# Kernel tuning notes

Hardware: AMD Instinct MI355X
Metric: run time of the kernel (lower is better)

The kernel has to match this reference:

```python
import jax, jax.numpy as jnp
import numpy as np

SEQ, D_IN, D_OUT = 4096, 1024, 1024


def setup_inputs() -> dict:
    key = jax.random.key(0)
    kx, kq, kk, kv = jax.random.split(key, 4)
    x = jax.random.normal(kx, (SEQ, D_IN), dtype=jnp.float32)
    # original uses torch.rand (uniform [0,1)) for parameter init
    W_query = jax.random.uniform(kq, (D_IN, D_OUT), dtype=jnp.float32)
    W_key = jax.random.uniform(kk, (D_IN, D_OUT), dtype=jnp.float32)
    W_value = jax.random.uniform(kv, (D_IN, D_OUT), dtype=jnp.float32)
    return {"x": x, "W_query": W_query, "W_key": W_key, "W_value": W_value}


def reference(x, W_query, W_key, W_value):
    queries = x @ W_query          # [S, d_out]
    keys = x @ W_key               # [S, d_out]
    values = x @ W_value           # [S, d_out]
    scale = keys.shape[-1] ** 0.5
    attn_scores = queries @ keys.T # [S, S]
    attn_weights = jax.nn.softmax(attn_scores / scale, axis=-1)
    context_vec = attn_weights @ values  # [S, d_out]
    return context_vec
```

## Files before the change

kernel.cpp:

```cpp
#include <hip/hip_runtime.h>
#include <stdint.h>

#define SEQ 4096
#define DM 1024

typedef __attribute__((ext_vector_type(8))) short short8;
typedef __attribute__((ext_vector_type(4))) float f32x4;
typedef unsigned short ushort_t;

__device__ inline ushort_t f2bf(float f) {
  union { float f; uint32_t u; } v; v.f = f;
  return (ushort_t)((v.u + 0x7FFFu + ((v.u >> 16) & 1u)) >> 16);
}
__device__ inline float bf2f(ushort_t h) {
  union { uint32_t u; float f; } v; v.u = ((uint32_t)h) << 16;
  return v.f;
}

__device__ inline void async_copy16(const void* g, void* lds) {
  __builtin_amdgcn_global_load_lds(
      (const __attribute__((address_space(1))) uint32_t*)g,
      (__attribute__((address_space(3))) uint32_t*)lds, 16, 0, 0);
}


__global__ __launch_bounds__(256, 3)
void gemm_qkv(const ushort_t* __restrict__ A, const ushort_t* __restrict__ Bt,
              ushort_t* __restrict__ Qb, ushort_t* __restrict__ Kb,
              ushort_t* __restrict__ Vb) {
  __shared__ ushort_t As[2][128 * 32];
  __shared__ ushort_t Bs[2][128 * 32];
  const int t = threadIdx.x;
  const int wave = t >> 6, lane = t & 63;
  const int quad = lane >> 4, l16 = lane & 15;
  const int m0 = blockIdx.y * 128, n0 = blockIdx.x * 128;
  const bool is_v = (n0 >= 2048);
  const int wm = (wave & 1) * 64, wn = (wave >> 1) * 64;
  const int srow = lane >> 2;
  const int sf = (srow >> 1) & 3;
  const int gcol = (((lane & 3) - sf) & 3) * 8;
  const int rf = (l16 >> 1) & 3;
  const int aslot = ((quad + rf) & 3) * 8;

  f32x4 acc[4][4] = {};

  for (int k0 = 0; k0 < 1024; k0 += 32) {
#pragma unroll
    for (int i = 0; i < 2; ++i) {
      int c = wave * 2 + i;
      const ushort_t* ga = A + (size_t)(m0 + c * 16 + srow) * 2048 + k0 + gcol;
      const ushort_t* gb = Bt + (size_t)(n0 + c * 16 + srow) * 2048 + k0 + gcol;
      async_copy16(ga, As[0] + c * 512);
      async_copy16(gb, Bs[0] + c * 512);
      if (!is_v) {
        async_copy16(ga + 1024, As[1] + c * 512);
        async_copy16(gb + 1024, Bs[1] + c * 512);
      }
    }
    __syncthreads();
    short8 a[4], b[4], x[4];
#pragma unroll
    for (int i = 0; i < 4; ++i) {
      a[i] = *(const short8*)(As[0] + (wm + i * 16 + l16) * 32 + aslot);
      b[i] = *(const short8*)(Bs[0] + (wn + i * 16 + l16) * 32 + aslot);
    }
#pragma unroll
    for (int i = 0; i < 4; ++i)
#pragma unroll
      for (int j = 0; j < 4; ++j)
        acc[i][j] = __builtin_amdgcn_mfma_f32_16x16x32_bf16(a[i], b[j], acc[i][j], 0, 0, 0);
    if (!is_v) {
#pragma unroll
      for (int j = 0; j < 4; ++j)
        x[j] = *(const short8*)(Bs[1] + (wn + j * 16 + l16) * 32 + aslot);
#pragma unroll
      for (int i = 0; i < 4; ++i)
#pragma unroll
        for (int j = 0; j < 4; ++j)
          acc[i][j] = __builtin_amdgcn_mfma_f32_16x16x32_bf16(a[i], x[j], acc[i][j], 0, 0, 0);
#pragma unroll
      for (int i = 0; i < 4; ++i)
        x[i] = *(const short8*)(As[1] + (wm + i * 16 + l16) * 32 + aslot);
#pragma unroll
      for (int i = 0; i < 4; ++i)
#pragma unroll
        for (int j = 0; j < 4; ++j)
          acc[i][j] = __builtin_amdgcn_mfma_f32_16x16x32_bf16(x[i], b[j], acc[i][j], 0, 0, 0);
    }
    __syncthreads();
  }

  if (is_v) {
    const int cb = n0 - 2048;
#pragma unroll
    for (int i = 0; i < 4; ++i)
#pragma unroll
      for (int j = 0; j < 4; ++j)
#pragma unroll
        for (int r = 0; r < 4; ++r) {
          int row = m0 + wm + i * 16 + quad * 4 + r;
          int col = cb + wn + j * 16 + l16;
          Vb[(size_t)row * 1024 + col] = f2bf(acc[i][j][r]);
        }
  } else {
    ushort_t* Cm = (n0 < 1024) ? Qb : Kb;
    const int cb = n0 & 1023;
#pragma unroll
    for (int i = 0; i < 4; ++i)
#pragma unroll
      for (int j = 0; j < 4; ++j)
#pragma unroll
        for (int r = 0; r < 4; ++r) {
          int row = m0 + wm + i * 16 + quad * 4 + r;
          int col = cb + wn + j * 16 + l16;
          float v = acc[i][j][r];
          ushort_t h = f2bf(v);
          size_t base = (size_t)row * 2048 + col;
          Cm[base] = h;
          Cm[base + 1024] = f2bf(v - bf2f(h));
        }
  }
}

__global__ __launch_bounds__(256, 3)
void gemm_sc(const ushort_t* __restrict__ A, const ushort_t* __restrict__ Bt,
             float* __restrict__ C, float scale) {
  const int id = blockIdx.x;
  const int rr = id & 7, w = (id >> 3) & 15, q = id >> 7;
  const int m0 = (q * 4 + (w >> 2)) * 128;
  const int n0 = (rr * 4 + (w & 3)) * 128;

  __shared__ ushort_t As[2][128 * 32];
  __shared__ ushort_t Bs[2][128 * 32];
  const int t = threadIdx.x;
  const int wave = t >> 6, lane = t & 63;
  const int quad = lane >> 4, l16 = lane & 15;
  const int wm = (wave & 1) * 64, wn = (wave >> 1) * 64;
  const int srow = lane >> 2;
  const int sf = (srow >> 1) & 3;
  const int gcol = (((lane & 3) - sf) & 3) * 8;
  const int rf = (l16 >> 1) & 3;
  const int aslot = ((quad + rf) & 3) * 8;

  f32x4 acc[4][4] = {};

  for (int k0 = 0; k0 < 1024; k0 += 32) {
#pragma unroll
    for (int i = 0; i < 2; ++i) {
      int c = wave * 2 + i;
      const ushort_t* ga = A + (size_t)(m0 + c * 16 + srow) * 2048 + k0 + gcol;
      const ushort_t* gb = Bt + (size_t)(n0 + c * 16 + srow) * 2048 + k0 + gcol;
      async_copy16(ga,        As[0] + c * 512);
      async_copy16(ga + 1024, As[1] + c * 512);
      async_copy16(gb,        Bs[0] + c * 512);
      async_copy16(gb + 1024, Bs[1] + c * 512);
    }
    __syncthreads();
    short8 a[4], b[4], x[4];
#pragma unroll
    for (int i = 0; i < 4; ++i) {
      a[i] = *(const short8*)(As[0] + (wm + i * 16 + l16) * 32 + aslot);
      b[i] = *(const short8*)(Bs[0] + (wn + i * 16 + l16) * 32 + aslot);
    }
#pragma unroll
    for (int i = 0; i < 4; ++i)
#pragma unroll
      for (int j = 0; j < 4; ++j)
        acc[i][j] = __builtin_amdgcn_mfma_f32_16x16x32_bf16(a[i], b[j], acc[i][j], 0, 0, 0);
#pragma unroll
    for (int j = 0; j < 4; ++j)
      x[j] = *(const short8*)(Bs[1] + (wn + j * 16 + l16) * 32 + aslot);
#pragma unroll
    for (int i = 0; i < 4; ++i)
#pragma unroll
      for (int j = 0; j < 4; ++j)
        acc[i][j] = __builtin_amdgcn_mfma_f32_16x16x32_bf16(a[i], x[j], acc[i][j], 0, 0, 0);
#pragma unroll
    for (int i = 0; i < 4; ++i)
      x[i] = *(const short8*)(As[1] + (wm + i * 16 + l16) * 32 + aslot);
#pragma unroll
    for (int i = 0; i < 4; ++i)
#pragma unroll
      for (int j = 0; j < 4; ++j)
        acc[i][j] = __builtin_amdgcn_mfma_f32_16x16x32_bf16(x[i], b[j], acc[i][j], 0, 0, 0);
    __syncthreads();
  }

#pragma unroll
  for (int i = 0; i < 4; ++i)
#pragma unroll
    for (int j = 0; j < 4; ++j)
#pragma unroll
      for (int r = 0; r < 4; ++r) {
        int row = m0 + wm + i * 16 + quad * 4 + r;
        int col = n0 + wn + j * 16 + l16;
        C[(size_t)row * SEQ + col] = acc[i][j][r] * scale;
      }
}

__global__ __launch_bounds__(256)
void gemm_pv(const ushort_t* __restrict__ P, const ushort_t* __restrict__ Vt,
             float* __restrict__ C) {
  const int id = blockIdx.x;
  const int g = ((id >> 6) << 3) | (id & 7);
  const int j = (id >> 3) & 7;
  const int z = g & 3, m = g >> 2;
  const int m0 = m * 128, n0 = j * 128, kbeg = z * 1024;

  __shared__ ushort_t As[128 * 32];
  __shared__ ushort_t Bs[128 * 32];
  const int t = threadIdx.x;
  const int wave = t >> 6, lane = t & 63;
  const int quad = lane >> 4, l16 = lane & 15;
  const int wm = (wave & 1) * 64, wn = (wave >> 1) * 64;
  const int srow = lane >> 2;
  const int sf = (srow >> 1) & 3;
  const int gcol = (((lane & 3) - sf) & 3) * 8;
  const int rf = (l16 >> 1) & 3;
  const int aslot = ((quad + rf) & 3) * 8;

  f32x4 acc[4][4] = {};
  for (int k0 = kbeg; k0 < kbeg + 1024; k0 += 32) {
#pragma unroll
    for (int i = 0; i < 2; ++i) {
      int c = wave * 2 + i;
      async_copy16(P + (size_t)(m0 + c * 16 + srow) * 4096 + k0 + gcol, As + c * 512);
      async_copy16(Vt + (size_t)(n0 + c * 16 + srow) * SEQ + k0 + gcol, Bs + c * 512);
    }
    __syncthreads();
    short8 a[4], b[4];
#pragma unroll
    for (int i = 0; i < 4; ++i) {
      a[i] = *(const short8*)(As + (wm + i * 16 + l16) * 32 + aslot);
      b[i] = *(const short8*)(Bs + (wn + i * 16 + l16) * 32 + aslot);
    }
#pragma unroll
    for (int i = 0; i < 4; ++i)
#pragma unroll
      for (int j2 = 0; j2 < 4; ++j2)
        acc[i][j2] = __builtin_amdgcn_mfma_f32_16x16x32_bf16(a[i], b[j2], acc[i][j2], 0, 0, 0);
    __syncthreads();
  }
#pragma unroll
  for (int i = 0; i < 4; ++i)
#pragma unroll
    for (int j2 = 0; j2 < 4; ++j2)
#pragma unroll
      for (int r = 0; r < 4; ++r) {
        int row = m0 + wm + i * 16 + quad * 4 + r;
        int col = n0 + wn + j2 * 16 + l16;
        atomicAdd(C + (size_t)row * DM + col, acc[i][j2][r]);
      }
}

__global__ __launch_bounds__(256)
void split_x(const float* __restrict__ x, ushort_t* __restrict__ Xp) {
  int idx = (blockIdx.x * 256 + threadIdx.x) * 4;
  int r = idx >> 10, c = idx & 1023;
  float4 v = *(const float4*)(x + idx);
  ushort4 hi, lo;
  hi.x = f2bf(v.x); lo.x = f2bf(v.x - bf2f(hi.x));
  hi.y = f2bf(v.y); lo.y = f2bf(v.y - bf2f(hi.y));
  hi.z = f2bf(v.z); lo.z = f2bf(v.z - bf2f(hi.z));
  hi.w = f2bf(v.w); lo.w = f2bf(v.w - bf2f(hi.w));
  *(ushort4*)(Xp + (size_t)r * 2048 + c) = hi;
  *(ushort4*)(Xp + (size_t)r * 2048 + 1024 + c) = lo;
}

__global__ __launch_bounds__(256)
void splitT_w(const float* __restrict__ W, ushort_t* __restrict__ Wp) {
  __shared__ float tile[64][65];
  const int bn = blockIdx.x * 64, bk = blockIdx.y * 64;
  const int tx = threadIdx.x & 63, ty = threadIdx.x >> 6;
#pragma unroll
  for (int i = ty; i < 64; i += 4)
    tile[i][tx] = W[(size_t)(bk + i) * DM + bn + tx];
  __syncthreads();
#pragma unroll
  for (int i = ty; i < 64; i += 4) {
    float v = tile[tx][i];
    ushort_t h = f2bf(v);
    Wp[(size_t)(bn + i) * 2048 + bk + tx] = h;
    Wp[(size_t)(bn + i) * 2048 + 1024 + bk + tx] = f2bf(v - bf2f(h));
  }
}

__global__ __launch_bounds__(256)
void transpose_bf16(const ushort_t* __restrict__ in, int istride,
                    ushort_t* __restrict__ out, int R) {
  __shared__ ushort_t tile[64][65];
  const int bc = blockIdx.x * 64, br = blockIdx.y * 64;
  const int tx = threadIdx.x & 63, ty = threadIdx.x >> 6;
#pragma unroll
  for (int i = ty; i < 64; i += 4)
    tile[i][tx] = in[(size_t)(br + i) * istride + bc + tx];
  __syncthreads();
#pragma unroll
  for (int i = ty; i < 64; i += 4)
    out[(size_t)(bc + i) * R + br + tx] = tile[tx][i];
}

__global__ __launch_bounds__(256)
void softmax_rows(const float* __restrict__ S, ushort_t* __restrict__ Pd) {
  const int row = blockIdx.x;
  const int t = threadIdx.x, lane = t & 63, wave = t >> 6;
  const float4* s4 = (const float4*)(S + (size_t)row * SEQ);
  float4 v[4];
  float m = -3.4e38f;
#pragma unroll
  for (int i = 0; i < 4; ++i) {
    v[i] = s4[i * 256 + t];
    m = fmaxf(m, fmaxf(fmaxf(v[i].x, v[i].y), fmaxf(v[i].z, v[i].w)));
  }
  __shared__ float redm[4], reds[4];
#pragma unroll
  for (int o = 32; o; o >>= 1) m = fmaxf(m, __shfl_xor(m, o));
  if (lane == 0) redm[wave] = m;
  __syncthreads();
  m = fmaxf(fmaxf(redm[0], redm[1]), fmaxf(redm[2], redm[3]));
  float sum = 0.f;
#pragma unroll
  for (int i = 0; i < 4; ++i) {
    v[i].x = __expf(v[i].x - m); v[i].y = __expf(v[i].y - m);
    v[i].z = __expf(v[i].z - m); v[i].w = __expf(v[i].w - m);
    sum += v[i].x + v[i].y + v[i].z + v[i].w;
  }
#pragma unroll
  for (int o = 32; o; o >>= 1) sum += __shfl_xor(sum, o);
  if (lane == 0) reds[wave] = sum;
  __syncthreads();
  const float inv = 1.f / (reds[0] + reds[1] + reds[2] + reds[3]);
  ushort4* p4 = (ushort4*)(Pd + (size_t)row * SEQ);
#pragma unroll
  for (int i = 0; i < 4; ++i) {
    ushort4 o;
    o.x = f2bf(v[i].x * inv); o.y = f2bf(v[i].y * inv);
    o.z = f2bf(v[i].z * inv); o.w = f2bf(v[i].w * inv);
    p4[i * 256 + t] = o;
  }
}

extern "C" void kernel_launch(void* const* d_in, const int* in_sizes, int n_in,
                              void* d_out, int out_size, void* d_ws, size_t ws_size,
                              hipStream_t stream) {
  const float* x  = (const float*)d_in[0];
  const float* Wq = (const float*)d_in[1];
  const float* Wk = (const float*)d_in[2];
  const float* Wv = (const float*)d_in[3];
  float* out = (float*)d_out;
  char* ws = (char*)d_ws;
  const size_t MB = (size_t)1 << 20;
  ushort_t* Xp   = (ushort_t*)(ws + 0 * MB);
  ushort_t* Wall = (ushort_t*)(ws + 16 * MB);
  ushort_t* Qb   = (ushort_t*)(ws + 28 * MB);
  ushort_t* Kb   = (ushort_t*)(ws + 44 * MB);
  ushort_t* Vb   = (ushort_t*)(ws + 60 * MB);
  ushort_t* VT   = (ushort_t*)(ws + 68 * MB);
  float*    S    = (float*)(ws + 76 * MB);
  ushort_t* Pd   = (ushort_t*)(ws + 0 * MB);

  hipMemsetAsync(d_out, 0, (size_t)SEQ * DM * sizeof(float), stream);

  split_x<<<SEQ * DM / 1024, 256, 0, stream>>>(x, Xp);
  splitT_w<<<dim3(16, 16), 256, 0, stream>>>(Wq, Wall + (size_t)0 * DM * 2048);
  splitT_w<<<dim3(16, 16), 256, 0, stream>>>(Wk, Wall + (size_t)1 * DM * 2048);
  splitT_w<<<dim3(16, 16), 256, 0, stream>>>(Wv, Wall + (size_t)2 * DM * 2048);

  gemm_qkv<<<dim3(3 * DM / 128, SEQ / 128), 256, 0, stream>>>(
      Xp, Wall, Qb, Kb, Vb);

  transpose_bf16<<<dim3(DM / 64, SEQ / 64), 256, 0, stream>>>(Vb, 1024, VT, SEQ);

  gemm_sc<<<1024, 256, 0, stream>>>(Qb, Kb, S, 0.03125f);

  softmax_rows<<<SEQ, 256, 0, stream>>>(S, Pd);

  gemm_pv<<<1024, 256, 0, stream>>>(Pd, VT, out);
}
```

Baseline: 364.3 us.

## Deepen PV k-tile to 64, merge weight split launches, simplify score-GEMM grid

The PV GEMM now stages 64-wide K tiles with an 8-slot XOR swizzle, so it does two MFMA sub-steps per barrier pair and needs half as many synchronizations. The three per-weight split/transpose launches are merged into a single launch using blockIdx.z. The score GEMM drops its swizzled block-to-tile mapping in favour of a plain 2D grid, which may lose L2 locality. The PV change doubles its LDS use per block, which could reduce occupancy.

```diff
diff --git a/kernel.cpp b/kernel.cpp
--- a/kernel.cpp
+++ b/kernel.cpp
@@ -125,10 +125,7 @@
 __global__ __launch_bounds__(256, 3)
 void gemm_sc(const ushort_t* __restrict__ A, const ushort_t* __restrict__ Bt,
              float* __restrict__ C, float scale) {
-  const int id = blockIdx.x;
-  const int rr = id & 7, w = (id >> 3) & 15, q = id >> 7;
-  const int m0 = (q * 4 + (w >> 2)) * 128;
-  const int n0 = (rr * 4 + (w & 3)) * 128;
+  const int m0 = blockIdx.y * 128, n0 = blockIdx.x * 128;
 
   __shared__ ushort_t As[2][128 * 32];
   __shared__ ushort_t Bs[2][128 * 32];
@@ -207,38 +204,42 @@
   const int z = g & 3, m = g >> 2;
   const int m0 = m * 128, n0 = j * 128, kbeg = z * 1024;
 
-  __shared__ ushort_t As[128 * 32];
-  __shared__ ushort_t Bs[128 * 32];
+  __shared__ ushort_t As[128 * 64];
+  __shared__ ushort_t Bs[128 * 64];
   const int t = threadIdx.x;
   const int wave = t >> 6, lane = t & 63;
   const int quad = lane >> 4, l16 = lane & 15;
   const int wm = (wave & 1) * 64, wn = (wave >> 1) * 64;
-  const int srow = lane >> 2;
-  const int sf = (srow >> 1) & 3;
-  const int gcol = (((lane & 3) - sf) & 3) * 8;
-  const int rf = (l16 >> 1) & 3;
-  const int aslot = ((quad + rf) & 3) * 8;
+  const int srow = lane >> 3;
+  const int gcol = (((lane & 7) - srow) & 7) * 8;
+  const int rs = l16 & 7;
 
   f32x4 acc[4][4] = {};
-  for (int k0 = kbeg; k0 < kbeg + 1024; k0 += 32) {
-#pragma unroll
-    for (int i = 0; i < 2; ++i) {
-      int c = wave * 2 + i;
-      async_copy16(P + (size_t)(m0 + c * 16 + srow) * 4096 + k0 + gcol, As + c * 512);
-      async_copy16(Vt + (size_t)(n0 + c * 16 + srow) * SEQ + k0 + gcol, Bs + c * 512);
-    }
-    __syncthreads();
-    short8 a[4], b[4];
+  for (int k0 = kbeg; k0 < kbeg + 1024; k0 += 64) {
 #pragma unroll
     for (int i = 0; i < 4; ++i) {
-      a[i] = *(const short8*)(As + (wm + i * 16 + l16) * 32 + aslot);
-      b[i] = *(const short8*)(Bs + (wn + i * 16 + l16) * 32 + aslot);
-    }
-#pragma unroll
-    for (int i = 0; i < 4; ++i)
-#pragma unroll
-      for (int j2 = 0; j2 < 4; ++j2)
-        acc[i][j2] = __builtin_amdgcn_mfma_f32_16x16x32_bf16(a[i], b[j2], acc[i][j2], 0, 0, 0);
+      int c = wave * 4 + i;
+      async_copy16(P + (size_t)(m0 + c * 8 + srow) * 4096 + k0 + gcol,
+                   As + c * 512);
+      async_copy16(Vt + (size_t)(n0 + c * 8 + srow) * SEQ + k0 + gcol,
+                   Bs + c * 512);
+    }
+    __syncthreads();
+#pragma unroll
+    for (int q = 0; q < 2; ++q) {
+      short8 a[4], b[4];
+#pragma unroll
+      for (int i = 0; i < 4; ++i) {
+        int slot = ((q * 4 + quad + rs) & 7) * 8;
+        a[i] = *(const short8*)(As + (wm + i * 16 + l16) * 64 + slot);
+        b[i] = *(const short8*)(Bs + (wn + i * 16 + l16) * 64 + slot);
+      }
+#pragma unroll
+      for (int i = 0; i < 4; ++i)
+#pragma unroll
+        for (int j2 = 0; j2 < 4; ++j2)
+          acc[i][j2] = __builtin_amdgcn_mfma_f32_16x16x32_bf16(a[i], b[j2], acc[i][j2], 0, 0, 0);
+    }
     __syncthreads();
   }
 #pragma unroll
@@ -268,7 +269,10 @@
 }
 
 __global__ __launch_bounds__(256)
-void splitT_w(const float* __restrict__ W, ushort_t* __restrict__ Wp) {
+void splitT_w3(const float* __restrict__ W0, const float* __restrict__ W1,
+               const float* __restrict__ W2, ushort_t* __restrict__ Wp) {
+  const float* W = (blockIdx.z == 0) ? W0 : (blockIdx.z == 1) ? W1 : W2;
+  ushort_t* Wo = Wp + (size_t)blockIdx.z * DM * 2048;
   __shared__ float tile[64][65];
   const int bn = blockIdx.x * 64, bk = blockIdx.y * 64;
   const int tx = threadIdx.x & 63, ty = threadIdx.x >> 6;
@@ -280,8 +284,8 @@
   for (int i = ty; i < 64; i += 4) {
     float v = tile[tx][i];
     ushort_t h = f2bf(v);
-    Wp[(size_t)(bn + i) * 2048 + bk + tx] = h;
-    Wp[(size_t)(bn + i) * 2048 + 1024 + bk + tx] = f2bf(v - bf2f(h));
+    Wo[(size_t)(bn + i) * 2048 + bk + tx] = h;
+    Wo[(size_t)(bn + i) * 2048 + 1024 + bk + tx] = f2bf(v - bf2f(h));
   }
 }
 
@@ -362,16 +366,14 @@
   hipMemsetAsync(d_out, 0, (size_t)SEQ * DM * sizeof(float), stream);
 
   split_x<<<SEQ * DM / 1024, 256, 0, stream>>>(x, Xp);
-  splitT_w<<<dim3(16, 16), 256, 0, stream>>>(Wq, Wall + (size_t)0 * DM * 2048);
-  splitT_w<<<dim3(16, 16), 256, 0, stream>>>(Wk, Wall + (size_t)1 * DM * 2048);
-  splitT_w<<<dim3(16, 16), 256, 0, stream>>>(Wv, Wall + (size_t)2 * DM * 2048);
+  splitT_w3<<<dim3(16, 16, 3), 256, 0, stream>>>(Wq, Wk, Wv, Wall);
 
   gemm_qkv<<<dim3(3 * DM / 128, SEQ / 128), 256, 0, stream>>>(
       Xp, Wall, Qb, Kb, Vb);
 
   transpose_bf16<<<dim3(DM / 64, SEQ / 64), 256, 0, stream>>>(Vb, 1024, VT, SEQ);
 
-  gemm_sc<<<1024, 256, 0, stream>>>(Qb, Kb, S, 0.03125f);
+  gemm_sc<<<dim3(SEQ / 128, SEQ / 128), 256, 0, stream>>>(Qb, Kb, S, 0.03125f);
 
   softmax_rows<<<SEQ, 256, 0, stream>>>(S, Pd);
 
```

Result: faster. 344.1 us (-5.5%).
